# Kernel optimization log

Measured on AMD Instinct MI355X. Metric: run time of the kernel, lower is better.

Reference implementation:

```python
import jax, jax.numpy as jnp
import numpy as np
import math

B, S, D, H = 2, 2048, 1024, 16
DH = D // H  # dim_per_head = 64


def setup_inputs() -> dict:
    key = jax.random.key(0)
    ks = jax.random.split(key, 12)
    s = 1.0 / math.sqrt(D)
    return {
        "key": jax.random.normal(ks[0], (B, S, D), jnp.float32),
        "value": jax.random.normal(ks[1], (B, S, D), jnp.float32),
        "query": jax.random.normal(ks[2], (B, S, D), jnp.float32),
        "mask": jax.random.randint(ks[3], (B, S, S), 0, 2).astype(bool),
        "Wq": jax.random.normal(ks[4], (D, D), jnp.float32) * s,
        "bq": jnp.zeros((D,), jnp.float32),
        "Wk": jax.random.normal(ks[5], (D, D), jnp.float32) * s,
        "bk": jnp.zeros((D,), jnp.float32),
        "Wv": jax.random.normal(ks[6], (D, D), jnp.float32) * s,
        "bv": jnp.zeros((D,), jnp.float32),
        "Wo": jax.random.normal(ks[7], (D, D), jnp.float32) * s,
        "bo": jnp.zeros((D,), jnp.float32),
    }


def _shape(x):
    # [B, S, D] -> [B, H, S, DH]
    return x.reshape(B, -1, H, DH).transpose(0, 2, 1, 3)


def reference(key, value, query, mask, Wq, bq, Wk, bk, Wv, bv, Wo, bo):
    q = _shape(query @ Wq.T + bq)  # [B,H,Sq,DH]
    k = _shape(key @ Wk.T + bk)    # [B,H,Sk,DH]
    v = _shape(value @ Wv.T + bv)  # [B,H,Sk,DH]
    q = q / jnp.sqrt(jnp.asarray(DH, q.dtype))
    scores = jnp.einsum("bhqd,bhkd->bhqk", q, k)
    scores = jnp.where(mask[:, None, :, :], jnp.asarray(-1e18, scores.dtype), scores)
    attn = jax.nn.softmax(scores, axis=-1)
    # dropout is identity in eval/deterministic reference
    ctx = jnp.einsum("bhqk,bhkd->bhqd", attn, v)
    ctx = ctx.transpose(0, 2, 1, 3).reshape(B, -1, D)  # unshape
    return ctx @ Wo.T + bo
```

## Files before the change

kernel.cpp:

```cpp
#include <hip/hip_runtime.h>
#include <math.h>


constexpr int Bc  = 2;
constexpr int Sc  = 2048;
constexpr int Dc  = 1024;
constexpr int Hc  = 16;
constexpr int DHc = 64;
constexpr int BSc = Bc * Sc;

constexpr float LOG2E = 1.4426950408889634f;

typedef __bf16 bf16x8 __attribute__((ext_vector_type(8)));
typedef __bf16 bf16x4 __attribute__((ext_vector_type(4)));
typedef __bf16 bf16x2 __attribute__((ext_vector_type(2)));
typedef float  f32x4  __attribute__((ext_vector_type(4)));
typedef float  f32x16 __attribute__((ext_vector_type(16)));
typedef unsigned uint32x2 __attribute__((ext_vector_type(2)));
typedef unsigned uint32x4 __attribute__((ext_vector_type(4)));

#define GLDS16(gp, lp) __builtin_amdgcn_global_load_lds( \
    (const __attribute__((address_space(1))) void*)(gp), \
    (__attribute__((address_space(3))) void*)(lp), 16, 0, 0)

__global__ __launch_bounds__(256)
void prep(const float* __restrict__ W0, const float* __restrict__ W1,
          const float* __restrict__ W2, const float* __restrict__ W3,
          __bf16* __restrict__ Whi,
          const float* __restrict__ A0, const float* __restrict__ A1,
          const float* __restrict__ A2, __bf16* __restrict__ Abf,
          const int* __restrict__ mask, unsigned long long* __restrict__ mpk)
{
    const int bid = blockIdx.x;
    const int tid = threadIdx.x;

    if (bid < 4096) {
        const float* src[4] = {W0, W1, W2, W3};
        const int z  = bid >> 10;
        const int bx = bid & 1023;
        const size_t idx = ((size_t)bx * 256 + tid) * 4;
        const float4 v = *(const float4*)&src[z][idx];
        bf16x4 o;
        o[0] = (__bf16)v.x; o[1] = (__bf16)v.y;
        o[2] = (__bf16)v.z; o[3] = (__bf16)v.w;
        *(bf16x4*)&Whi[(size_t)z * Dc * Dc + idx] = o;
    } else if (bid < 10240) {
        const float* src[3] = {A0, A1, A2};
        const int lin = bid - 4096;
        const int z  = lin >> 11;
        const int bx = lin & 2047;
        const size_t idx = ((size_t)bx * 256 + tid) * 8;
        const float4 a = *(const float4*)&src[z][idx];
        const float4 b = *(const float4*)&src[z][idx + 4];
        bf16x8 o;
        o[0] = (__bf16)a.x; o[1] = (__bf16)a.y; o[2] = (__bf16)a.z; o[3] = (__bf16)a.w;
        o[4] = (__bf16)b.x; o[5] = (__bf16)b.y; o[6] = (__bf16)b.z; o[7] = (__bf16)b.w;
        *(bf16x8*)&Abf[(size_t)z * BSc * Dc + idx] = o;
    } else {
        const int bx   = bid - 10240;
        const int lane = tid & 63;
        const size_t waveBase = ((size_t)bx * 4 + (tid >> 6)) * 256;
        unsigned long long b0 = __ballot(mask[waveBase + lane]        != 0);
        unsigned long long b1 = __ballot(mask[waveBase + 64 + lane]   != 0);
        unsigned long long b2 = __ballot(mask[waveBase + 128 + lane]  != 0);
        unsigned long long b3 = __ballot(mask[waveBase + 192 + lane]  != 0);
        if (lane == 0) {
            unsigned long long* dst = mpk + (waveBase >> 6);
            dst[0] = b0; dst[1] = b1; dst[2] = b2; dst[3] = b3;
        }
    }
}

template<int KD>
__device__ __forceinline__ void sweep128bb(const __bf16* __restrict__ A,
                                           const __bf16* __restrict__ Wh,
                                           char* AsB, char* WsB,
                                           int gm0, int gn0, f32x4 acc[4][4])
{
    const int tid  = threadIdx.x;
    const int w    = tid >> 6;
    const int lane = tid & 63;
    const int cc   = lane & 15;
    const int g    = lane >> 4;
    const int wm   = (w & 1) * 64;
    const int wn   = (w >> 1) * 64;

    int wrow[4], wchk[4];
#pragma unroll
    for (int r = 0; r < 4; ++r) {
        const int L = r * 256 + tid;
        wrow[r] = L >> 3;
        wchk[r] = (L & 7) ^ (wrow[r] & 7);
    }

#pragma unroll
    for (int r = 0; r < 4; ++r) {
        GLDS16(Wh + (size_t)(gn0 + wrow[r]) * KD + wchk[r] * 8,
               WsB + (r * 256 + tid) * 16);
        GLDS16(A + (size_t)(gm0 + wrow[r]) * KD + wchk[r] * 8,
               AsB + (r * 256 + tid) * 16);
    }

    for (int it = 0; it < KD / 64; ++it) {
        const char* As = AsB + (it & 1) * 16384;
        const char* Ws = WsB + (it & 1) * 16384;
        __syncthreads();

        if (it + 1 < KD / 64) {
            const int kn = (it + 1) * 64;
            char* Wn = WsB + ((it + 1) & 1) * 16384;
            char* An = AsB + ((it + 1) & 1) * 16384;
#pragma unroll
            for (int r = 0; r < 4; ++r) {
                GLDS16(Wh + (size_t)(gn0 + wrow[r]) * KD + kn + wchk[r] * 8,
                       Wn + (r * 256 + tid) * 16);
                GLDS16(A + (size_t)(gm0 + wrow[r]) * KD + kn + wchk[r] * 8,
                       An + (r * 256 + tid) * 16);
            }
        }

        __builtin_amdgcn_s_setprio(1);
#pragma unroll
        for (int kk = 0; kk < 2; ++kk) {
            const int cb4 = (kk * 4 + g) << 4;
            bf16x8 af[4], bfr[4];
#pragma unroll
            for (int mt = 0; mt < 4; ++mt) {
                const int row = wm + mt * 16 + cc;
                af[mt] = *(const bf16x8*)(As + row * 128 + (cb4 ^ ((row & 7) << 4)));
            }
#pragma unroll
            for (int nt = 0; nt < 4; ++nt) {
                const int row = wn + nt * 16 + cc;
                bfr[nt] = *(const bf16x8*)(Ws + row * 128 + (cb4 ^ ((row & 7) << 4)));
            }
#pragma unroll
            for (int mt = 0; mt < 4; ++mt)
#pragma unroll
                for (int nt = 0; nt < 4; ++nt)
                    acc[mt][nt] = __builtin_amdgcn_mfma_f32_16x16x32_bf16(
                        af[mt], bfr[nt], acc[mt][nt], 0, 0, 0);
        }
        __builtin_amdgcn_s_setprio(0);
    }
}

__device__ __forceinline__ void sweep64p(const __bf16* __restrict__ Ahi,
                                         const __bf16* __restrict__ Alo,
                                         const __bf16* __restrict__ Wh,
                                         char* WsB, char* AhB, char* AlB,
                                         int gm0, int gn0, f32x4 acc[2][4])
{
    const int tid  = threadIdx.x;
    const int w    = tid >> 6;
    const int lane = tid & 63;
    const int cc   = lane & 15;
    const int g    = lane >> 4;
    const int wm   = (w & 1) * 32;
    const int wn   = (w >> 1) * 64;

    int wrow[4], wchk[4];
#pragma unroll
    for (int r = 0; r < 4; ++r) {
        const int L = r * 256 + tid;
        wrow[r] = L >> 3;
        wchk[r] = (L & 7) ^ (wrow[r] & 7);
    }
    int arow[2], achk[2];
#pragma unroll
    for (int r = 0; r < 2; ++r) {
        const int L = r * 256 + tid;
        arow[r] = L >> 3;
        achk[r] = (L & 7) ^ (arow[r] & 7);
    }

#pragma unroll
    for (int r = 0; r < 4; ++r)
        GLDS16(Wh + (size_t)(gn0 + wrow[r]) * Dc + wchk[r] * 8,
               WsB + (r * 256 + tid) * 16);
#pragma unroll
    for (int r = 0; r < 2; ++r) {
        GLDS16(Ahi + (size_t)(gm0 + arow[r]) * Dc + achk[r] * 8,
               AhB + (r * 256 + tid) * 16);
        GLDS16(Alo + (size_t)(gm0 + arow[r]) * Dc + achk[r] * 8,
               AlB + (r * 256 + tid) * 16);
    }

    for (int it = 0; it < Dc / 64; ++it) {
        const char* Ws = WsB + (it & 1) * 16384;
        const char* Ah = AhB + (it & 1) * 8192;
        const char* Al = AlB + (it & 1) * 8192;
        __syncthreads();

        if (it + 1 < Dc / 64) {
            const int kn = (it + 1) * 64;
            char* Wn = WsB + ((it + 1) & 1) * 16384;
            char* Hn = AhB + ((it + 1) & 1) * 8192;
            char* Ln = AlB + ((it + 1) & 1) * 8192;
#pragma unroll
            for (int r = 0; r < 4; ++r)
                GLDS16(Wh + (size_t)(gn0 + wrow[r]) * Dc + kn + wchk[r] * 8,
                       Wn + (r * 256 + tid) * 16);
#pragma unroll
            for (int r = 0; r < 2; ++r) {
                GLDS16(Ahi + (size_t)(gm0 + arow[r]) * Dc + kn + achk[r] * 8,
                       Hn + (r * 256 + tid) * 16);
                GLDS16(Alo + (size_t)(gm0 + arow[r]) * Dc + kn + achk[r] * 8,
                       Ln + (r * 256 + tid) * 16);
            }
        }

        __builtin_amdgcn_s_setprio(1);
#pragma unroll
        for (int kk = 0; kk < 2; ++kk) {
            const int cb4 = (kk * 4 + g) << 4;
            bf16x8 ahi[2], alo[2], bfr[4];
#pragma unroll
            for (int mt = 0; mt < 2; ++mt) {
                const int row = wm + mt * 16 + cc;
                const int off = row * 128 + (cb4 ^ ((row & 7) << 4));
                ahi[mt] = *(const bf16x8*)(Ah + off);
                alo[mt] = *(const bf16x8*)(Al + off);
            }
#pragma unroll
            for (int nt = 0; nt < 4; ++nt) {
                const int row = wn + nt * 16 + cc;
                bfr[nt] = *(const bf16x8*)(Ws + row * 128 + (cb4 ^ ((row & 7) << 4)));
            }
#pragma unroll
            for (int mt = 0; mt < 2; ++mt)
#pragma unroll
                for (int nt = 0; nt < 4; ++nt) {
                    acc[mt][nt] = __builtin_amdgcn_mfma_f32_16x16x32_bf16(
                        ahi[mt], bfr[nt], acc[mt][nt], 0, 0, 0);
                    acc[mt][nt] = __builtin_amdgcn_mfma_f32_16x16x32_bf16(
                        alo[mt], bfr[nt], acc[mt][nt], 0, 0, 0);
                }
        }
        __builtin_amdgcn_s_setprio(0);
    }
}

__global__ __launch_bounds__(256)
void qkv_mfma(const __bf16* __restrict__ Abf, const __bf16* __restrict__ Whi,
              const float* __restrict__ bq, const float* __restrict__ bk,
              const float* __restrict__ bv,
              __bf16* __restrict__ Qo, __bf16* __restrict__ Ko, __bf16* __restrict__ Vt)
{
    __shared__ __align__(16) char smem[65536];

    const int z = blockIdx.y;
    const float* bias = (z == 0) ? bq : (z == 1) ? bk : bv;
    const float scale = (z == 0) ? 0.125f * LOG2E : 1.0f;
    const __bf16* A   = Abf + (size_t)z * BSc * Dc;
    const __bf16* Wh  = Whi + (size_t)z * Dc * Dc;

    const int lb  = (blockIdx.x & 7) * 32 + (blockIdx.x >> 3);
    const int idx = lb & 31;
    const int gm0 = ((lb >> 5) * 4 + (idx & 3)) * 128;
    const int gn0 = (idx >> 2) * 128;

    f32x4 acc[4][4];
#pragma unroll
    for (int mt = 0; mt < 4; ++mt)
#pragma unroll
        for (int nt = 0; nt < 4; ++nt) acc[mt][nt] = {0.f, 0.f, 0.f, 0.f};

    sweep128bb<Dc>(A, Wh, smem, smem + 32768, gm0, gn0, acc);

    const int tid = threadIdx.x;
    const int w = tid >> 6, lane = tid & 63;
    const int cc = lane & 15, g = lane >> 4;
    const int wm = (w & 1) * 64, wn = (w >> 1) * 64;

    float bias4[4];
#pragma unroll
    for (int nt = 0; nt < 4; ++nt) bias4[nt] = bias[gn0 + wn + nt * 16 + cc];

    if (z == 2) {
#pragma unroll
        for (int mt = 0; mt < 4; ++mt)
#pragma unroll
            for (int nt = 0; nt < 4; ++nt) {
                const int col = gn0 + wn + nt * 16 + cc;
                const int h = col >> 6, dh = col & 63;
                const int row0 = gm0 + wm + mt * 16 + g * 4;
                const int b = row0 >> 11, s0 = row0 & 2047;
                bf16x4 vv;
#pragma unroll
                for (int reg = 0; reg < 4; ++reg)
                    vv[reg] = (__bf16)(acc[mt][nt][reg] + bias4[nt]);
                *(bf16x4*)&Vt[(((size_t)(b * Hc + h)) * DHc + dh) * Sc + s0] = vv;
            }
    } else {
        __bf16* O = (z == 0) ? Qo : Ko;
#pragma unroll
        for (int mt = 0; mt < 4; ++mt)
#pragma unroll
            for (int nt = 0; nt < 4; ++nt) {
                const int col = gn0 + wn + nt * 16 + cc;
                const int h = col >> 6, dh = col & 63;
#pragma unroll
                for (int reg = 0; reg < 4; ++reg) {
                    const int row = gm0 + wm + mt * 16 + g * 4 + reg;
                    const int b = row >> 11, s = row & 2047;
                    O[(((size_t)(b * Hc + h)) * Sc + s) * DHc + dh] =
                        (__bf16)((acc[mt][nt][reg] + bias4[nt]) * scale);
                }
            }
    }
}

__global__ __launch_bounds__(256)
void out_mfma(const __bf16* __restrict__ ctxHi, const __bf16* __restrict__ ctxLo,
              const __bf16* __restrict__ Wohi,
              const float* __restrict__ bo, float* __restrict__ out)
{
    __shared__ __align__(16) char smem[65536];

    const int lb = (blockIdx.x & 7) * 64 + (blockIdx.x >> 3);
    const int gm0 = ((lb >> 6) * 8 + (lb & 7)) * 64;
    const int gn0 = ((lb >> 3) & 7) * 128;

    f32x4 acc[2][4];
#pragma unroll
    for (int mt = 0; mt < 2; ++mt)
#pragma unroll
        for (int nt = 0; nt < 4; ++nt) acc[mt][nt] = {0.f, 0.f, 0.f, 0.f};

    sweep64p(ctxHi, ctxLo, Wohi, smem, smem + 32768, smem + 49152, gm0, gn0, acc);

    const int tid = threadIdx.x;
    const int w = tid >> 6, lane = tid & 63;
    const int cc = lane & 15, g = lane >> 4;
    const int wm = (w & 1) * 32, wn = (w >> 1) * 64;

    float bias4[4];
#pragma unroll
    for (int nt = 0; nt < 4; ++nt) bias4[nt] = bo[gn0 + wn + nt * 16 + cc];

#pragma unroll
    for (int mt = 0; mt < 2; ++mt)
#pragma unroll
        for (int nt = 0; nt < 4; ++nt) {
            const int col = gn0 + wn + nt * 16 + cc;
#pragma unroll
            for (int reg = 0; reg < 4; ++reg) {
                const int row = gm0 + wm + mt * 16 + g * 4 + reg;
                out[(size_t)row * Dc + col] = acc[mt][nt][reg] + bias4[nt];
            }
        }
}

__device__ __forceinline__ void stage_pair(const __bf16* Kb, const __bf16* Vtb,
                                           char* H, int t0,
                                           int rowi0, int ski0, int ci0,
                                           int rowi1, int ski1, int ci1)
{
#pragma unroll
    for (int s = 0; s < 2; ++s) {
        char* B = H + s * 16384;
        const int kn = (t0 + s) * 64;
        GLDS16(Kb + (size_t)(kn + rowi0) * DHc + ski0 * 8, B + ci0 * 16);
        GLDS16(Vtb + (size_t)rowi0 * Sc + kn + ski0 * 8, B + 8192 + ci0 * 16);
        GLDS16(Kb + (size_t)(kn + rowi1) * DHc + ski1 * 8, B + ci1 * 16);
        GLDS16(Vtb + (size_t)rowi1 * Sc + kn + ski1 * 8, B + 8192 + ci1 * 16);
    }
}

__device__ __forceinline__ void tile_step(const char* Ks, const char* Vs,
                                          const bf16x8 qa[4], const f32x16& zb,
                                          unsigned long long mw, int c, int u,
                                          float lp[4], f32x16 o[2])
{
    f32x16 sc[2];
    __builtin_amdgcn_s_setprio(1);
#pragma unroll
    for (int nt = 0; nt < 2; ++nt) {
        const int row = nt * 32 + c;
        const int rx  = (row & 7) << 4;
        const bf16x8 kb0 = *(const bf16x8*)(Ks + row * 128 + ((u * 16) ^ rx));
        f32x16 z = __builtin_amdgcn_mfma_f32_32x32x16_bf16(kb0, qa[0], zb, 0, 0, 0);
#pragma unroll
        for (int ch = 1; ch < 4; ++ch) {
            const bf16x8 kb = *(const bf16x8*)
                (Ks + row * 128 + ((ch * 32 + u * 16) ^ rx));
            z = __builtin_amdgcn_mfma_f32_32x32x16_bf16(kb, qa[ch], z, 0, 0, 0);
        }
        sc[nt] = z;
    }
    __builtin_amdgcn_s_setprio(0);

    unsigned pk[2][4][2];
#pragma unroll
    for (int nt = 0; nt < 2; ++nt)
#pragma unroll
        for (int rr = 0; rr < 4; ++rr) {
            const unsigned nib =
                (unsigned)(mw >> (nt * 32 + rr * 8 + u * 4)) & 0xFu;
            float pv[4];
#pragma unroll
            for (int r = 0; r < 4; ++r) {
                float p = __builtin_amdgcn_exp2f(sc[nt][rr * 4 + r]);
                p = (nib & (1u << r)) ? 0.f : p;
                lp[rr] += p;
                pv[r] = p;
            }
            bf16x2 t0; t0[0] = (__bf16)pv[0]; t0[1] = (__bf16)pv[1];
            bf16x2 t1; t1[0] = (__bf16)pv[2]; t1[1] = (__bf16)pv[3];
            pk[nt][rr][0] = __builtin_bit_cast(unsigned, t0);
            pk[nt][rr][1] = __builtin_bit_cast(unsigned, t1);
        }

    bf16x8 pa[4];
#pragma unroll
    for (int kc = 0; kc < 4; ++kc) {
        const int nt = kc >> 1;
        const int r0 = (kc & 1) * 2;
        uint32x2 w0 = __builtin_amdgcn_permlane32_swap(
            pk[nt][r0][0], pk[nt][r0 + 1][0], false, false);
        uint32x2 w1 = __builtin_amdgcn_permlane32_swap(
            pk[nt][r0][1], pk[nt][r0 + 1][1], false, false);
        uint32x4 wds;
        wds[0] = w0[0]; wds[1] = w1[0]; wds[2] = w0[1]; wds[3] = w1[1];
        pa[kc] = __builtin_bit_cast(bf16x8, wds);
    }

    __builtin_amdgcn_s_setprio(1);
#pragma unroll
    for (int dt = 0; dt < 2; ++dt) {
        const int row = dt * 32 + c;
        const int rx  = (row & 7) << 4;
#pragma unroll
        for (int kc = 0; kc < 4; ++kc) {
            const bf16x8 vb = *(const bf16x8*)
                (Vs + row * 128 + ((kc * 32 + u * 16) ^ rx));
            o[dt] = __builtin_amdgcn_mfma_f32_32x32x16_bf16(pa[kc], vb, o[dt], 0, 0, 0);
        }
    }
    __builtin_amdgcn_s_setprio(0);
}

__global__ __launch_bounds__(256, 2)
void attn_mfma(const __bf16* __restrict__ Q, const __bf16* __restrict__ K,
               const __bf16* __restrict__ Vt,
               const unsigned long long* __restrict__ mp,
               __bf16* __restrict__ ctxHi, __bf16* __restrict__ ctxLo)
{
    __shared__ __align__(16) char smem[65536];

    const int tid  = threadIdx.x;
    const int w    = tid >> 6;
    const int lane = tid & 63;
    const int c    = lane & 31;
    const int u    = lane >> 5;
    const int bh   = blockIdx.y;
    const int b    = bh >> 4;
    const int h    = bh & 15;
    const int qw   = blockIdx.x * 128 + w * 32;

    const __bf16* Qb  = Q  + (size_t)bh * Sc * DHc;
    const __bf16* Kb  = K  + (size_t)bh * Sc * DHc;
    const __bf16* Vtb = Vt + (size_t)bh * DHc * Sc;

    bf16x8 qa[4];
#pragma unroll
    for (int ch = 0; ch < 4; ++ch)
        qa[ch] = *(const bf16x8*)&Qb[(size_t)(qw + c) * DHc + ch * 16 + u * 8];

    f32x16 o[2], zb;
#pragma unroll
    for (int i = 0; i < 16; ++i) { o[0][i] = 0.f; o[1][i] = 0.f; zb[i] = -24.f; }
    float lp[4] = {0.f, 0.f, 0.f, 0.f};

    const int ci0 = tid,        ci1 = 256 + tid;
    const int rowi0 = ci0 >> 3, rowi1 = ci1 >> 3;
    const int ski0 = (ci0 & 7) ^ (rowi0 & 7);
    const int ski1 = (ci1 & 7) ^ (rowi1 & 7);

    const size_t mbase = ((size_t)(b * Sc + qw + c) << 5);

    stage_pair(Kb, Vtb, smem, 0, rowi0, ski0, ci0, rowi1, ski1, ci1);

    for (int j = 0; j < 16; ++j) {
        __syncthreads();
        if (j + 1 < 16)
            stage_pair(Kb, Vtb, smem + ((j + 1) & 1) * 32768, 2 * j + 2,
                       rowi0, ski0, ci0, rowi1, ski1, ci1);

        const char* H = smem + (j & 1) * 32768;
        const unsigned long long mw0 = mp[mbase + 2 * j];
        const unsigned long long mw1 = mp[mbase + 2 * j + 1];

        tile_step(H,         H + 8192,  qa, zb, mw0, c, u, lp, o);
        tile_step(H + 16384, H + 24576, qa, zb, mw1, c, u, lp, o);
    }

    float lsum = (lp[0] + lp[1]) + (lp[2] + lp[3]);
    lsum += __shfl_xor(lsum, 32);
    const float linv = 1.0f / lsum;

    float inv[16];
#pragma unroll
    for (int i = 0; i < 16; ++i)
        inv[i] = __shfl(linv, (i & 3) + 8 * (i >> 2) + 4 * u);

#pragma unroll
    for (int dt = 0; dt < 2; ++dt)
#pragma unroll
        for (int i = 0; i < 16; ++i) {
            const int q = qw + (i & 3) + 8 * (i >> 2) + 4 * u;
            const size_t idx = ((size_t)b * Sc + q) * Dc + h * 64 + dt * 32 + c;
            const float v = o[dt][i] * inv[i];
            const __bf16 hi = (__bf16)v;
            ctxHi[idx] = hi;
            ctxLo[idx] = (__bf16)(v - (float)hi);
        }
}

extern "C" void kernel_launch(void* const* d_in, const int* in_sizes, int n_in,
                              void* d_out, int out_size, void* d_ws, size_t ws_size,
                              hipStream_t stream)
{
    const float* key   = (const float*)d_in[0];
    const float* value = (const float*)d_in[1];
    const float* query = (const float*)d_in[2];
    const int*   mask  = (const int*)  d_in[3];
    const float* Wq    = (const float*)d_in[4];
    const float* bq    = (const float*)d_in[5];
    const float* Wk    = (const float*)d_in[6];
    const float* bk    = (const float*)d_in[7];
    const float* Wv    = (const float*)d_in[8];
    const float* bv    = (const float*)d_in[9];
    const float* Wo    = (const float*)d_in[10];
    const float* bo    = (const float*)d_in[11];
    float* out = (float*)d_out;

    char* wsb = (char*)d_ws;
    __bf16* Qbf  = (__bf16*)(wsb);
    __bf16* Kbf  = (__bf16*)(wsb + ((size_t)8  << 20));
    __bf16* Vt   = (__bf16*)(wsb + ((size_t)16 << 20));
    unsigned long long* mpk = (unsigned long long*)(wsb + ((size_t)32 << 20));
    __bf16* Whi  = (__bf16*)(wsb + ((size_t)33 << 20));
    __bf16* ctxHi = (__bf16*)(wsb + ((size_t)41 << 20));
    __bf16* ctxLo = (__bf16*)(wsb + ((size_t)49 << 20));
    __bf16* Abf  = (__bf16*)(wsb + ((size_t)57 << 20));

    prep<<<dim3(18432), 256, 0, stream>>>(Wq, Wk, Wv, Wo, Whi,
                                          query, key, value, Abf,
                                          mask, mpk);

    dim3 gqkv(256, 3);
    qkv_mfma<<<gqkv, 256, 0, stream>>>(Abf, Whi, bq, bk, bv, Qbf, Kbf, Vt);

    dim3 gattn(Sc / 128, Bc * Hc);
    attn_mfma<<<gattn, 256, 0, stream>>>(Qbf, Kbf, Vt, mpk, ctxHi, ctxLo);

    out_mfma<<<dim3(512), 256, 0, stream>>>(ctxHi, ctxLo, Whi + (size_t)3 * Dc * Dc,
                                            bo, out);
}
```

Measured before the change: 247.9 us.

## Double attention block to 8 waves with XCD-aware block remapping

The attention kernel now launches 256 blocks of 512 threads, each covering 256 query rows, instead of 512 blocks of 256 threads covering 128. Each staged K/V tile is shared by twice as many waves, and each thread issues half as many global-to-LDS loads. Block indices are remapped so that the 32 blocks sent to each XCD group heads together, which should improve L2 reuse of K/V. The trade-off is one block per CU with 64KB LDS and fewer blocks in flight, which may hurt latency hiding and load balance.

```diff
diff --git a/kernel.cpp b/kernel.cpp
--- a/kernel.cpp
+++ b/kernel.cpp
@@ -352,19 +352,16 @@
         }
 }
 
-__device__ __forceinline__ void stage_pair(const __bf16* Kb, const __bf16* Vtb,
-                                           char* H, int t0,
-                                           int rowi0, int ski0, int ci0,
-                                           int rowi1, int ski1, int ci1)
+__device__ __forceinline__ void stage_pair512(const __bf16* Kb, const __bf16* Vtb,
+                                              char* H, int t0,
+                                              int rowi, int ski, int ci)
 {
 #pragma unroll
     for (int s = 0; s < 2; ++s) {
         char* B = H + s * 16384;
         const int kn = (t0 + s) * 64;
-        GLDS16(Kb + (size_t)(kn + rowi0) * DHc + ski0 * 8, B + ci0 * 16);
-        GLDS16(Vtb + (size_t)rowi0 * Sc + kn + ski0 * 8, B + 8192 + ci0 * 16);
-        GLDS16(Kb + (size_t)(kn + rowi1) * DHc + ski1 * 8, B + ci1 * 16);
-        GLDS16(Vtb + (size_t)rowi1 * Sc + kn + ski1 * 8, B + 8192 + ci1 * 16);
+        GLDS16(Kb + (size_t)(kn + rowi) * DHc + ski * 8, B + ci * 16);
+        GLDS16(Vtb + (size_t)rowi * Sc + kn + ski * 8, B + 8192 + ci * 16);
     }
 }
 
@@ -441,7 +438,7 @@
     __builtin_amdgcn_s_setprio(0);
 }
 
-__global__ __launch_bounds__(256, 2)
+__global__ __launch_bounds__(512, 1)
 void attn_mfma(const __bf16* __restrict__ Q, const __bf16* __restrict__ K,
                const __bf16* __restrict__ Vt,
                const unsigned long long* __restrict__ mp,
@@ -454,10 +451,15 @@
     const int lane = tid & 63;
     const int c    = lane & 31;
     const int u    = lane >> 5;
-    const int bh   = blockIdx.y;
-    const int b    = bh >> 4;
-    const int h    = bh & 15;
-    const int qw   = blockIdx.x * 128 + w * 32;
+
+    const int bx  = blockIdx.x;
+    const int lb  = (bx & 7) * 32 + (bx >> 3);
+    const int i5  = lb & 31;
+    const int bh  = (lb >> 5) * 4 + (i5 >> 3);
+    const int qb  = i5 & 7;
+    const int b   = bh >> 4;
+    const int h   = bh & 15;
+    const int qw  = qb * 256 + w * 32;
 
     const __bf16* Qb  = Q  + (size_t)bh * Sc * DHc;
     const __bf16* Kb  = K  + (size_t)bh * Sc * DHc;
@@ -473,20 +475,18 @@
     for (int i = 0; i < 16; ++i) { o[0][i] = 0.f; o[1][i] = 0.f; zb[i] = -24.f; }
     float lp[4] = {0.f, 0.f, 0.f, 0.f};
 
-    const int ci0 = tid,        ci1 = 256 + tid;
-    const int rowi0 = ci0 >> 3, rowi1 = ci1 >> 3;
-    const int ski0 = (ci0 & 7) ^ (rowi0 & 7);
-    const int ski1 = (ci1 & 7) ^ (rowi1 & 7);
+    const int rowi = tid >> 3;
+    const int ski  = (tid & 7) ^ (rowi & 7);
 
     const size_t mbase = ((size_t)(b * Sc + qw + c) << 5);
 
-    stage_pair(Kb, Vtb, smem, 0, rowi0, ski0, ci0, rowi1, ski1, ci1);
+    stage_pair512(Kb, Vtb, smem, 0, rowi, ski, tid);
 
     for (int j = 0; j < 16; ++j) {
         __syncthreads();
         if (j + 1 < 16)
-            stage_pair(Kb, Vtb, smem + ((j + 1) & 1) * 32768, 2 * j + 2,
-                       rowi0, ski0, ci0, rowi1, ski1, ci1);
+            stage_pair512(Kb, Vtb, smem + ((j + 1) & 1) * 32768, 2 * j + 2,
+                          rowi, ski, tid);
 
         const char* H = smem + (j & 1) * 32768;
         const unsigned long long mw0 = mp[mbase + 2 * j];
@@ -553,8 +553,7 @@
     dim3 gqkv(256, 3);
     qkv_mfma<<<gqkv, 256, 0, stream>>>(Abf, Whi, bq, bk, bv, Qbf, Kbf, Vt);
 
-    dim3 gattn(Sc / 128, Bc * Hc);
-    attn_mfma<<<gattn, 256, 0, stream>>>(Qbf, Kbf, Vt, mpk, ctxHi, ctxLo);
+    attn_mfma<<<dim3(256), 512, 0, stream>>>(Qbf, Kbf, Vt, mpk, ctxHi, ctxLo);
 
     out_mfma<<<dim3(512), 256, 0, stream>>>(ctxHi, ctxLo, Whi + (size_t)3 * Dc * Dc,
                                             bo, out);
```

Result: no change. 248.7 us (+0.3%).
